# Kernel tuning notes

Measured on AMD Instinct MI355X. Metric: run time of the kernel, lower is better.

Reference implementation:

```python
import jax, jax.numpy as jnp
import numpy as np

B, S, D, DK, DV = 4, 4096, 1024, 64, 64


def setup_inputs() -> dict:
    rng = jax.random.key(0)
    k1, k2, k3, k4, k5, k6 = jax.random.split(rng, 6)
    query = jax.random.normal(k1, (B, S, D), dtype=jnp.float32)
    key = jax.random.normal(k2, (B, S, D), dtype=jnp.float32)
    value = jax.random.normal(k3, (B, S, D), dtype=jnp.float32)
    Wq = jax.random.normal(k4, (D, DK), dtype=jnp.float32)
    Wk = jax.random.normal(k5, (D, DK), dtype=jnp.float32)
    Wv = jax.random.normal(k6, (D, DV), dtype=jnp.float32)
    mask = jnp.tril(jnp.ones((S, S), dtype=jnp.bool_))  # causal mask, broadcasts over batch
    return {"query": query, "key": key, "value": value,
            "Wq": Wq, "Wk": Wk, "Wv": Wv, "mask": mask}


def reference(query, key, value, Wq, Wk, Wv, mask):
    # linear projections: [B,S,D] @ [D,dk] -> [B,S,dk]
    q = jnp.matmul(query, Wq)
    k = jnp.matmul(key, Wk)
    v = jnp.matmul(value, Wv)
    scale = 1.0 / jnp.sqrt(jnp.asarray(DK, dtype=q.dtype))
    # scores: [B,S,S]
    attn = jnp.einsum("bqd,bkd->bqk", q, k) * scale
    attn = jnp.where(mask, attn, -jnp.inf)  # mask==0 -> -inf
    attn = jax.nn.softmax(attn, axis=-1)
    x = jnp.matmul(attn, v)  # [B,S,dv]
    return x
```

## Files before the change

kernel.cpp:

```cpp
#include <hip/hip_runtime.h>
#include <math.h>


#define SEQ 4096
#define DIM 1024
#define HD  64
#define NB  4
#define NSPLIT 4

typedef __attribute__((ext_vector_type(4))) float    f32x4;
typedef __attribute__((ext_vector_type(8))) _Float16 f16x8;
typedef __attribute__((ext_vector_type(4))) _Float16 f16x4;

#define MFMA16 __builtin_amdgcn_mfma_f32_16x16x32_f16

__device__ __forceinline__ int SW(int row, int k) {
  return row * 64 + (k ^ ((row & 7) << 3));
}

#define GLD16(dst, ptr, imm)                                        \
  asm volatile("global_load_dwordx4 %0, %1, off offset:" #imm      \
               : "=&v"(dst) : "v"(ptr))

#define VMWAIT(n)                                                   \
  do {                                                              \
    asm volatile("s_waitcnt vmcnt(" #n ")" ::: "memory");           \
    __builtin_amdgcn_sched_barrier(0);                              \
  } while (0)

__global__ __launch_bounds__(256) void wsplit_kernel(
    const float* __restrict__ Wq, const float* __restrict__ Wk,
    const float* __restrict__ Wv, _Float16* __restrict__ wf)
{
  const int which = blockIdx.x;
  const int kt    = blockIdx.y;
  const float* __restrict__ W = (which == 0) ? Wq : (which == 1) ? Wk : Wv;
  const float scale = (which == 0) ? 0.18033688011112042f : 1.0f;
  const size_t tb = ((size_t)which * 16 + kt) * 8192;
#pragma unroll
  for (int i = 0; i < 2; ++i) {
    const int pair = threadIdx.x + 256 * i;
    const int lane = pair & 63, f = pair >> 6;
    const int ks = f >> 2, ct = f & 3;
    const int col = ct * 16 + (lane & 15);
    const int k0 = kt * 64 + ks * 32 + (lane >> 4) * 8;
    f16x8 hv, lv;
#pragma unroll
    for (int j = 0; j < 8; ++j) {
      const float y = W[(size_t)(k0 + j) * HD + col] * scale;
      const _Float16 h = (_Float16)y;
      hv[j] = h;
      lv[j] = (_Float16)(y - (float)h);
    }
    *(f16x8*)&wf[tb + (size_t)f * 512 + lane * 8]       = hv;
    *(f16x8*)&wf[tb + (size_t)(8 + f) * 512 + lane * 8] = lv;
  }
}

__global__ __launch_bounds__(64, 2) void proj_kernel(
    const float* __restrict__ Xq, const float* __restrict__ Xk,
    const float* __restrict__ Xv,
    const _Float16* __restrict__ wf,
    _Float16* __restrict__ qh, _Float16* __restrict__ ql,
    _Float16* __restrict__ kh, _Float16* __restrict__ kl,
    _Float16* __restrict__ vt)
{
  const int which = blockIdx.y;
  const float* __restrict__ X = (which == 0) ? Xq : (which == 1) ? Xk : Xv;

  const int lane = threadIdx.x & 63;
  const int bm = blockIdx.x * 16;

  const float* xp = X + (size_t)(bm + (lane & 15)) * DIM + ((lane >> 4) * 8);
  const _Float16* wp = wf + (size_t)which * 131072 + lane * 8;

  f32x4 acc[4] = {{0,0,0,0},{0,0,0,0},{0,0,0,0},{0,0,0,0}};

  f32x4 xA[4], xB[4];
  f16x8 whA[8], wlA[8], whB[8], wlB[8];

#define LOADT(xs, whs, wls, kt)                                      \
  do {                                                               \
    const float* xb = xp + (kt) * 64;                                \
    GLD16(xs[0], xb, 0);                                             \
    GLD16(xs[1], xb, 16);                                            \
    GLD16(xs[2], xb, 128);                                           \
    GLD16(xs[3], xb, 144);                                           \
    const _Float16* wb0 = wp + (size_t)(kt) * 8192;                  \
    const _Float16* wb1 = wb0 + 2048;                                \
    const _Float16* wb2 = wb0 + 4096;                                \
    const _Float16* wb3 = wb0 + 6144;                                \
    GLD16(whs[0], wb0, 0);                                           \
    GLD16(whs[1], wb0, 1024);                                        \
    GLD16(whs[2], wb0, 2048);                                        \
    GLD16(whs[3], wb0, 3072);                                        \
    GLD16(whs[4], wb1, 0);                                           \
    GLD16(whs[5], wb1, 1024);                                        \
    GLD16(whs[6], wb1, 2048);                                        \
    GLD16(whs[7], wb1, 3072);                                        \
    GLD16(wls[0], wb2, 0);                                           \
    GLD16(wls[1], wb2, 1024);                                        \
    GLD16(wls[2], wb2, 2048);                                        \
    GLD16(wls[3], wb2, 3072);                                        \
    GLD16(wls[4], wb3, 0);                                           \
    GLD16(wls[5], wb3, 1024);                                        \
    GLD16(wls[6], wb3, 2048);                                        \
    GLD16(wls[7], wb3, 3072);                                        \
  } while (0)

#define COMPUTET(xs, whs, wls)                                            \
  do {                                                                    \
    _Pragma("unroll")                                                     \
    for (int ks = 0; ks < 2; ++ks) {                                      \
      f16x8 xh, xl;                                                       \
      _Pragma("unroll")                                                   \
      for (int j = 0; j < 4; ++j) {                                       \
        const float v0 = xs[2 * ks][j];                                   \
        const _Float16 h0 = (_Float16)v0;                                 \
        xh[j] = h0; xl[j] = (_Float16)(v0 - (float)h0);                   \
        const float v1 = xs[2 * ks + 1][j];                               \
        const _Float16 h1 = (_Float16)v1;                                 \
        xh[j + 4] = h1; xl[j + 4] = (_Float16)(v1 - (float)h1);           \
      }                                                                   \
      _Pragma("unroll")                                                   \
      for (int ct = 0; ct < 4; ++ct) {                                    \
        acc[ct] = MFMA16(xh, whs[ks * 4 + ct], acc[ct], 0, 0, 0);         \
        acc[ct] = MFMA16(xl, whs[ks * 4 + ct], acc[ct], 0, 0, 0);         \
        acc[ct] = MFMA16(xh, wls[ks * 4 + ct], acc[ct], 0, 0, 0);         \
      }                                                                   \
    }                                                                     \
  } while (0)

  LOADT(xA, whA, wlA, 0);
  LOADT(xB, whB, wlB, 1);

#pragma unroll 1
  for (int kt = 0; kt < 14; kt += 2) {
    VMWAIT(20);
    COMPUTET(xA, whA, wlA);
    LOADT(xA, whA, wlA, kt + 2);
    VMWAIT(20);
    COMPUTET(xB, whB, wlB);
    LOADT(xB, whB, wlB, kt + 3);
  }
  VMWAIT(20);
  COMPUTET(xA, whA, wlA);
  VMWAIT(0);
  COMPUTET(xB, whB, wlB);
#undef LOADT
#undef COMPUTET

  const size_t orow0 = (size_t)bm + (lane >> 4) * 4;
  if (which < 2) {
    _Float16* oh = (which == 0) ? qh : kh;
    _Float16* ol = (which == 0) ? ql : kl;
#pragma unroll
    for (int ct = 0; ct < 4; ++ct)
#pragma unroll
      for (int r = 0; r < 4; ++r) {
        const float y = acc[ct][r];
        const _Float16 h = (_Float16)y;
        const size_t idx = (orow0 + r) * HD + ct * 16 + (lane & 15);
        oh[idx] = h;
        ol[idx] = (_Float16)(y - (float)h);
      }
  } else {
    const int batch = (int)(orow0 >> 12);
    const int pos = (int)(orow0 & 4095);
#pragma unroll
    for (int ct = 0; ct < 4; ++ct) {
      f16x4 hv;
#pragma unroll
      for (int r = 0; r < 4; ++r) hv[r] = (_Float16)acc[ct][r];
      *(f16x4*)&vt[((size_t)batch * HD + ct * 16 + (lane & 15)) * SEQ + pos] = hv;
    }
  }
}

__global__ __launch_bounds__(256) void attn_kernel(
    const _Float16* __restrict__ qh, const _Float16* __restrict__ ql,
    const _Float16* __restrict__ kh, const _Float16* __restrict__ kl,
    const _Float16* __restrict__ vt,
    _Float16* __restrict__ opart, float* __restrict__ mlp)
{
  __shared__ __attribute__((aligned(16))) _Float16 Ksh[64 * 64];
  __shared__ __attribute__((aligned(16))) _Float16 Ksl[64 * 64];
  __shared__ __attribute__((aligned(16))) _Float16 Vs [64 * 64];
  __shared__ __attribute__((aligned(16))) _Float16 Pt [64 * 64];

  const int t = threadIdx.x, lane = t & 63, w = t >> 6;
  const int b = blockIdx.y;
  const int p = blockIdx.x >> 2, s = blockIdx.x & 3;
  const size_t bS = (size_t)b * SEQ;

  for (int sel = 0; sel < 2; ++sel) {
    const int qb = sel ? (63 - p) : p;
    const int qrow0 = qb * 64 + w * 16;
    const int nt = (qb >= s) ? ((qb - s) >> 2) + 1 : 0;

    float m[4] = {-INFINITY, -INFINITY, -INFINITY, -INFINITY};
    float lsum[4] = {0.f, 0.f, 0.f, 0.f};
    f32x4 o[4] = {{0,0,0,0},{0,0,0,0},{0,0,0,0},{0,0,0,0}};

    if (nt > 0) {
      const _Float16* qhp = qh + (bS + qrow0 + (lane & 15)) * HD + ((lane >> 4) * 8);
      const _Float16* qlp = ql + (bS + qrow0 + (lane & 15)) * HD + ((lane >> 4) * 8);
      f16x8 qhf[2], qlf[2];
      qhf[0] = *(const f16x8*)(qhp);      qhf[1] = *(const f16x8*)(qhp + 32);
      qlf[0] = *(const f16x8*)(qlp);      qlf[1] = *(const f16x8*)(qlp + 32);

      for (int i = 0; i < nt; ++i) {
        const int kt = s + 4 * i;
        const int j0 = kt * 64;

        __syncthreads();
#pragma unroll
        for (int c = 0; c < 2; ++c) {
          const int lin = t + 256 * c;
          const int row = lin >> 3, d8 = (lin & 7) * 8;
          const int dst = SW(row, d8);
          *(f16x8*)&Ksh[dst] = *(const f16x8*)&kh[(bS + j0 + row) * HD + d8];
          *(f16x8*)&Ksl[dst] = *(const f16x8*)&kl[(bS + j0 + row) * HD + d8];
          *(f16x8*)&Vs[dst]  = *(const f16x8*)&vt[((size_t)b * HD + row) * SEQ + j0 + d8];
        }
        __syncthreads();

        f32x4 sacc[4] = {{0,0,0,0},{0,0,0,0},{0,0,0,0},{0,0,0,0}};
#pragma unroll
        for (int ks = 0; ks < 2; ++ks)
#pragma unroll
          for (int kt4 = 0; kt4 < 4; ++kt4) {
            const int ba = SW(kt4 * 16 + (lane & 15), ks * 32 + (lane >> 4) * 8);
            f16x8 bh = *(const f16x8*)&Ksh[ba];
            f16x8 bl = *(const f16x8*)&Ksl[ba];
            sacc[kt4] = MFMA16(qhf[ks], bh, sacc[kt4], 0, 0, 0);
            sacc[kt4] = MFMA16(qlf[ks], bh, sacc[kt4], 0, 0, 0);
            sacc[kt4] = MFMA16(qhf[ks], bl, sacc[kt4], 0, 0, 0);
          }

        if (kt == qb) {
#pragma unroll
          for (int kt4 = 0; kt4 < 4; ++kt4) {
            const int key = j0 + kt4 * 16 + (lane & 15);
#pragma unroll
            for (int r = 0; r < 4; ++r)
              if (key > qrow0 + (lane >> 4) * 4 + r) sacc[kt4][r] = -INFINITY;
          }
        }

        float alf[4];
#pragma unroll
        for (int r = 0; r < 4; ++r) {
          float mx = fmaxf(fmaxf(sacc[0][r], sacc[1][r]),
                           fmaxf(sacc[2][r], sacc[3][r]));
          mx = fmaxf(mx, __shfl_xor(mx, 1));
          mx = fmaxf(mx, __shfl_xor(mx, 2));
          mx = fmaxf(mx, __shfl_xor(mx, 4));
          mx = fmaxf(mx, __shfl_xor(mx, 8));
          const float mn = fmaxf(m[r], mx);
          const float al = exp2f(m[r] - mn);
          const int prow = w * 16 + (lane >> 4) * 4 + r;
          float ps = 0.f;
#pragma unroll
          for (int kt4 = 0; kt4 < 4; ++kt4) {
            const _Float16 ph = (_Float16)exp2f(sacc[kt4][r] - mn);
            ps += (float)ph;
            Pt[SW(prow, kt4 * 16 + (lane & 15))] = ph;
          }
          ps += __shfl_xor(ps, 1);
          ps += __shfl_xor(ps, 2);
          ps += __shfl_xor(ps, 4);
          ps += __shfl_xor(ps, 8);
          lsum[r] = lsum[r] * al + ps;
          m[r] = mn;
          alf[r] = al;
        }
        const f32x4 av = {alf[0], alf[1], alf[2], alf[3]};
#pragma unroll
        for (int ct = 0; ct < 4; ++ct) o[ct] *= av;

#pragma unroll
        for (int ks = 0; ks < 2; ++ks) {
          f16x8 pa = *(const f16x8*)&Pt[SW(w * 16 + (lane & 15),
                                           ks * 32 + (lane >> 4) * 8)];
#pragma unroll
          for (int ct = 0; ct < 4; ++ct) {
            f16x8 vb = *(const f16x8*)&Vs[SW(ct * 16 + (lane & 15),
                                             ks * 32 + (lane >> 4) * 8)];
            o[ct] = MFMA16(pa, vb, o[ct], 0, 0, 0);
          }
        }
      }
    }

    f32x4 invv;
#pragma unroll
    for (int r = 0; r < 4; ++r) invv[r] = (nt > 0) ? 1.0f / lsum[r] : 0.0f;
    const size_t ridx0 = (size_t)(b * NSPLIT + s) * SEQ + qrow0 + (lane >> 4) * 4;
#pragma unroll
    for (int ct = 0; ct < 4; ++ct)
#pragma unroll
      for (int r = 0; r < 4; ++r)
        opart[(ridx0 + r) * HD + ct * 16 + (lane & 15)] =
            (_Float16)(o[ct][r] * invv[r]);
    if ((lane & 15) == 0) {
#pragma unroll
      for (int r = 0; r < 4; ++r) {
        mlp[(ridx0 + r) * 2]     = m[r];
        mlp[(ridx0 + r) * 2 + 1] = lsum[r];
      }
    }
  }
}

__global__ __launch_bounds__(256) void combine_kernel(
    const _Float16* __restrict__ opart, const float* __restrict__ mlp,
    float* __restrict__ out)
{
  const int g = blockIdx.x * 256 + threadIdx.x;
  const int row = g >> 4;
  const int cq = (g & 15) * 4;
  const int b = row >> 12, pos = row & 4095;

  float mv[4], lv[4], msx = -INFINITY;
#pragma unroll
  for (int s = 0; s < 4; ++s) {
    const size_t ri = (size_t)(b * NSPLIT + s) * SEQ + pos;
    mv[s] = mlp[ri * 2];
    lv[s] = mlp[ri * 2 + 1];
    msx = fmaxf(msx, mv[s]);
  }
  f32x4 num = {0.f, 0.f, 0.f, 0.f};
  float L = 0.f;
#pragma unroll
  for (int s = 0; s < 4; ++s) {
    const float wgt = lv[s] * exp2f(mv[s] - msx);
    L += wgt;
    const size_t ri = (size_t)(b * NSPLIT + s) * SEQ + pos;
    const f16x4 ov = *(const f16x4*)&opart[ri * HD + cq];
#pragma unroll
    for (int j = 0; j < 4; ++j) num[j] += wgt * (float)ov[j];
  }
  const float inv = 1.0f / L;
  f32x4 res = {num[0] * inv, num[1] * inv, num[2] * inv, num[3] * inv};
  *(f32x4*)&out[(size_t)row * HD + cq] = res;
}

extern "C" void kernel_launch(void* const* d_in, const int* in_sizes, int n_in,
                              void* d_out, int out_size, void* d_ws, size_t ws_size,
                              hipStream_t stream) {
  const float* query = (const float*)d_in[0];
  const float* key   = (const float*)d_in[1];
  const float* value = (const float*)d_in[2];
  const float* Wq    = (const float*)d_in[3];
  const float* Wk    = (const float*)d_in[4];
  const float* Wv    = (const float*)d_in[5];

  float* out = (float*)d_out;

  _Float16* qh  = (_Float16*)d_ws;
  _Float16* ql  = qh  + (size_t)NB * SEQ * HD;
  _Float16* kh  = ql  + (size_t)NB * SEQ * HD;
  _Float16* kl  = kh  + (size_t)NB * SEQ * HD;
  _Float16* vt  = kl  + (size_t)NB * SEQ * HD;
  _Float16* wf  = vt  + (size_t)NB * SEQ * HD;
  _Float16* opart = wf + (size_t)3 * 16 * 8192;
  float* mlp = (float*)(opart + (size_t)NB * NSPLIT * SEQ * HD);

  wsplit_kernel<<<dim3(3, 16), 256, 0, stream>>>(Wq, Wk, Wv, wf);
  proj_kernel<<<dim3(1024, 3), 64, 0, stream>>>(query, key, value, wf,
                                                qh, ql, kh, kl, vt);
  attn_kernel<<<dim3(128, NB), 256, 0, stream>>>(qh, ql, kh, kl, vt, opart, mlp);
  combine_kernel<<<1024, 256, 0, stream>>>(opart, mlp, out);
}
```

Before: 108.8 us.

## Split projection K dimension in two and add finish kernel for reduction and layout

The projection GEMM is split along the reduction dimension into two halves, each writing fp32 partial sums, and uses 256-thread blocks of four waves instead of single-wave blocks. A new finish kernel sums the two partials, performs the hi/lo fp16 split for Q/K, and transposes V through shared memory so the vt writes are vectorised. The aim is more parallelism and shorter serial K loops in the projection, plus coalesced V-transpose stores. In exchange it adds an extra kernel launch and an fp32 partial-sum round trip through global memory.

```diff
diff --git a/kernel.cpp b/kernel.cpp
--- a/kernel.cpp
+++ b/kernel.cpp
@@ -14,10 +14,6 @@
 
 #define MFMA16 __builtin_amdgcn_mfma_f32_16x16x32_f16
 
-__device__ __forceinline__ int SW(int row, int k) {
-  return row * 64 + (k ^ ((row & 7) << 3));
-}
-
 #define GLD16(dst, ptr, imm)                                        \
   asm volatile("global_load_dwordx4 %0, %1, off offset:" #imm      \
                : "=&v"(dst) : "v"(ptr))
@@ -27,6 +23,10 @@
     asm volatile("s_waitcnt vmcnt(" #n ")" ::: "memory");           \
     __builtin_amdgcn_sched_barrier(0);                              \
   } while (0)
+
+__device__ __forceinline__ int SW(int row, int k) {
+  return row * 64 + (k ^ ((row & 7) << 3));
+}
 
 __global__ __launch_bounds__(256) void wsplit_kernel(
     const float* __restrict__ Wq, const float* __restrict__ Wk,
@@ -57,19 +57,19 @@
   }
 }
 
-__global__ __launch_bounds__(64, 2) void proj_kernel(
+__global__ __launch_bounds__(256, 2) void proj_kernel(
     const float* __restrict__ Xq, const float* __restrict__ Xk,
     const float* __restrict__ Xv,
     const _Float16* __restrict__ wf,
-    _Float16* __restrict__ qh, _Float16* __restrict__ ql,
-    _Float16* __restrict__ kh, _Float16* __restrict__ kl,
-    _Float16* __restrict__ vt)
+    float* __restrict__ Yp)
 {
-  const int which = blockIdx.y;
+  const int which = blockIdx.z;
+  const int ks    = blockIdx.y;
   const float* __restrict__ X = (which == 0) ? Xq : (which == 1) ? Xk : Xv;
 
-  const int lane = threadIdx.x & 63;
-  const int bm = blockIdx.x * 16;
+  const int t = threadIdx.x, lane = t & 63, w = t >> 6;
+  const int bm = blockIdx.x * 64 + w * 16;
+  const int kbase = ks * 8;
 
   const float* xp = X + (size_t)(bm + (lane & 15)) * DIM + ((lane >> 4) * 8);
   const _Float16* wp = wf + (size_t)which * 131072 + lane * 8;
@@ -111,37 +111,37 @@
 #define COMPUTET(xs, whs, wls)                                            \
   do {                                                                    \
     _Pragma("unroll")                                                     \
-    for (int ks = 0; ks < 2; ++ks) {                                      \
+    for (int kk = 0; kk < 2; ++kk) {                                      \
       f16x8 xh, xl;                                                       \
       _Pragma("unroll")                                                   \
       for (int j = 0; j < 4; ++j) {                                       \
-        const float v0 = xs[2 * ks][j];                                   \
+        const float v0 = xs[2 * kk][j];                                   \
         const _Float16 h0 = (_Float16)v0;                                 \
         xh[j] = h0; xl[j] = (_Float16)(v0 - (float)h0);                   \
-        const float v1 = xs[2 * ks + 1][j];                               \
+        const float v1 = xs[2 * kk + 1][j];                               \
         const _Float16 h1 = (_Float16)v1;                                 \
         xh[j + 4] = h1; xl[j + 4] = (_Float16)(v1 - (float)h1);           \
       }                                                                   \
       _Pragma("unroll")                                                   \
       for (int ct = 0; ct < 4; ++ct) {                                    \
-        acc[ct] = MFMA16(xh, whs[ks * 4 + ct], acc[ct], 0, 0, 0);         \
-        acc[ct] = MFMA16(xl, whs[ks * 4 + ct], acc[ct], 0, 0, 0);         \
-        acc[ct] = MFMA16(xh, wls[ks * 4 + ct], acc[ct], 0, 0, 0);         \
+        acc[ct] = MFMA16(xh, whs[kk * 4 + ct], acc[ct], 0, 0, 0);         \
+        acc[ct] = MFMA16(xl, whs[kk * 4 + ct], acc[ct], 0, 0, 0);         \
+        acc[ct] = MFMA16(xh, wls[kk * 4 + ct], acc[ct], 0, 0, 0);         \
       }                                                                   \
     }                                                                     \
   } while (0)
 
-  LOADT(xA, whA, wlA, 0);
-  LOADT(xB, whB, wlB, 1);
+  LOADT(xA, whA, wlA, kbase);
+  LOADT(xB, whB, wlB, kbase + 1);
 
 #pragma unroll 1
-  for (int kt = 0; kt < 14; kt += 2) {
+  for (int kt = 0; kt < 6; kt += 2) {
     VMWAIT(20);
     COMPUTET(xA, whA, wlA);
-    LOADT(xA, whA, wlA, kt + 2);
+    LOADT(xA, whA, wlA, kbase + kt + 2);
     VMWAIT(20);
     COMPUTET(xB, whB, wlB);
-    LOADT(xB, whB, wlB, kt + 3);
+    LOADT(xB, whB, wlB, kbase + kt + 3);
   }
   VMWAIT(20);
   COMPUTET(xA, whA, wlA);
@@ -151,29 +151,72 @@
 #undef COMPUTET
 
   const size_t orow0 = (size_t)bm + (lane >> 4) * 4;
+  float* yb = Yp + ((size_t)(ks * 3 + which) * SEQ * NB) * HD;
+#pragma unroll
+  for (int ct = 0; ct < 4; ++ct)
+#pragma unroll
+    for (int r = 0; r < 4; ++r)
+      yb[(orow0 + r) * HD + ct * 16 + (lane & 15)] = acc[ct][r];
+}
+
+__global__ __launch_bounds__(256) void finish_kernel(
+    const float* __restrict__ Yp,
+    _Float16* __restrict__ qh, _Float16* __restrict__ ql,
+    _Float16* __restrict__ kh, _Float16* __restrict__ kl,
+    _Float16* __restrict__ vt)
+{
+  __shared__ float Vs[64 * 65];
+  const int which = blockIdx.y;
+  const int t = threadIdx.x;
+  const int row = t >> 2;
+  const int c0 = (t & 3) * 16;
+  const size_t rbase = (size_t)blockIdx.x * 64;
+  const float* y0 = Yp + ((size_t)(0 * 3 + which) * SEQ * NB) * HD;
+  const float* y1 = Yp + ((size_t)(1 * 3 + which) * SEQ * NB) * HD;
+
+  float s[16];
+#pragma unroll
+  for (int u = 0; u < 4; ++u) {
+    const size_t off = (rbase + row) * HD + c0 + u * 4;
+    f32x4 a = *(const f32x4*)(y0 + off);
+    f32x4 b = *(const f32x4*)(y1 + off);
+#pragma unroll
+    for (int j = 0; j < 4; ++j) s[u * 4 + j] = a[j] + b[j];
+  }
+
   if (which < 2) {
     _Float16* oh = (which == 0) ? qh : kh;
     _Float16* ol = (which == 0) ? ql : kl;
-#pragma unroll
-    for (int ct = 0; ct < 4; ++ct)
-#pragma unroll
-      for (int r = 0; r < 4; ++r) {
-        const float y = acc[ct][r];
-        const _Float16 h = (_Float16)y;
-        const size_t idx = (orow0 + r) * HD + ct * 16 + (lane & 15);
-        oh[idx] = h;
-        ol[idx] = (_Float16)(y - (float)h);
-      }
+    f16x8 hv0, hv1, lv0, lv1;
+#pragma unroll
+    for (int j = 0; j < 8; ++j) {
+      const _Float16 h0 = (_Float16)s[j];
+      hv0[j] = h0; lv0[j] = (_Float16)(s[j] - (float)h0);
+      const _Float16 h1 = (_Float16)s[8 + j];
+      hv1[j] = h1; lv1[j] = (_Float16)(s[8 + j] - (float)h1);
+    }
+    const size_t ob = (rbase + row) * HD + c0;
+    *(f16x8*)&oh[ob]     = hv0;
+    *(f16x8*)&oh[ob + 8] = hv1;
+    *(f16x8*)&ol[ob]     = lv0;
+    *(f16x8*)&ol[ob + 8] = lv1;
   } else {
-    const int batch = (int)(orow0 >> 12);
-    const int pos = (int)(orow0 & 4095);
-#pragma unroll
-    for (int ct = 0; ct < 4; ++ct) {
-      f16x4 hv;
-#pragma unroll
-      for (int r = 0; r < 4; ++r) hv[r] = (_Float16)acc[ct][r];
-      *(f16x4*)&vt[((size_t)batch * HD + ct * 16 + (lane & 15)) * SEQ + pos] = hv;
+#pragma unroll
+    for (int j = 0; j < 16; ++j) Vs[row * 65 + c0 + j] = s[j];
+    __syncthreads();
+    const int col = t >> 2;
+    const int p0 = (t & 3) * 16;
+    const int b = (int)(rbase >> 12);
+    const int pos = (int)(rbase & 4095) + p0;
+    f16x8 o0, o1;
+#pragma unroll
+    for (int j = 0; j < 8; ++j) {
+      o0[j] = (_Float16)Vs[(p0 + j) * 65 + col];
+      o1[j] = (_Float16)Vs[(p0 + 8 + j) * 65 + col];
     }
+    _Float16* vb = vt + ((size_t)b * HD + col) * SEQ + pos;
+    *(f16x8*)(vb)     = o0;
+    *(f16x8*)(vb + 8) = o1;
   }
 }
 
@@ -227,15 +270,15 @@
 
         f32x4 sacc[4] = {{0,0,0,0},{0,0,0,0},{0,0,0,0},{0,0,0,0}};
 #pragma unroll
-        for (int ks = 0; ks < 2; ++ks)
+        for (int kk = 0; kk < 2; ++kk)
 #pragma unroll
           for (int kt4 = 0; kt4 < 4; ++kt4) {
-            const int ba = SW(kt4 * 16 + (lane & 15), ks * 32 + (lane >> 4) * 8);
+            const int ba = SW(kt4 * 16 + (lane & 15), kk * 32 + (lane >> 4) * 8);
             f16x8 bh = *(const f16x8*)&Ksh[ba];
             f16x8 bl = *(const f16x8*)&Ksl[ba];
-            sacc[kt4] = MFMA16(qhf[ks], bh, sacc[kt4], 0, 0, 0);
-            sacc[kt4] = MFMA16(qlf[ks], bh, sacc[kt4], 0, 0, 0);
-            sacc[kt4] = MFMA16(qhf[ks], bl, sacc[kt4], 0, 0, 0);
+            sacc[kt4] = MFMA16(qhf[kk], bh, sacc[kt4], 0, 0, 0);
+            sacc[kt4] = MFMA16(qlf[kk], bh, sacc[kt4], 0, 0, 0);
+            sacc[kt4] = MFMA16(qhf[kk], bl, sacc[kt4], 0, 0, 0);
           }
 
         if (kt == qb) {
@@ -280,13 +323,13 @@
         for (int ct = 0; ct < 4; ++ct) o[ct] *= av;
 
 #pragma unroll
-        for (int ks = 0; ks < 2; ++ks) {
+        for (int kk = 0; kk < 2; ++kk) {
           f16x8 pa = *(const f16x8*)&Pt[SW(w * 16 + (lane & 15),
-                                           ks * 32 + (lane >> 4) * 8)];
+                                           kk * 32 + (lane >> 4) * 8)];
 #pragma unroll
           for (int ct = 0; ct < 4; ++ct) {
             f16x8 vb = *(const f16x8*)&Vs[SW(ct * 16 + (lane & 15),
-                                             ks * 32 + (lane >> 4) * 8)];
+                                             kk * 32 + (lane >> 4) * 8)];
             o[ct] = MFMA16(pa, vb, o[ct], 0, 0, 0);
           }
         }
@@ -366,10 +409,11 @@
   _Float16* wf  = vt  + (size_t)NB * SEQ * HD;
   _Float16* opart = wf + (size_t)3 * 16 * 8192;
   float* mlp = (float*)(opart + (size_t)NB * NSPLIT * SEQ * HD);
+  float* Yp  = mlp + (size_t)NB * NSPLIT * SEQ * 2;
 
   wsplit_kernel<<<dim3(3, 16), 256, 0, stream>>>(Wq, Wk, Wv, wf);
-  proj_kernel<<<dim3(1024, 3), 64, 0, stream>>>(query, key, value, wf,
-                                                qh, ql, kh, kl, vt);
+  proj_kernel<<<dim3(256, 2, 3), 256, 0, stream>>>(query, key, value, wf, Yp);
+  finish_kernel<<<dim3(256, 3), 256, 0, stream>>>(Yp, qh, ql, kh, kl, vt);
   attn_kernel<<<dim3(128, NB), 256, 0, stream>>>(qh, ql, kh, kl, vt, opart, mlp);
   combine_kernel<<<1024, 256, 0, stream>>>(opart, mlp, out);
 }
```

New measurement: 114.2 us. 4.9% more time.
